# Kernel tuning notes

Hardware: AMD Instinct MI355X
Metric: run time of the kernel (lower is better)

## Reference

```python
import jax, jax.numpy as jnp
import numpy as np


def setup_inputs() -> dict:
    key = jax.random.key(0)
    ks = jax.random.split(key, 8)
    bs, slen, d = 16, 2048, 1024
    scale = 1.0 / np.sqrt(d)
    return {
        "query": jax.random.normal(ks[0], (bs, d), jnp.float32),
        "states": jax.random.normal(ks[1], (bs, slen, d), jnp.float32),
        "Wq": jax.random.normal(ks[2], (d, d), jnp.float32) * scale,
        "bq": jax.random.normal(ks[3], (d,), jnp.float32) * 0.01,
        "Wk": jax.random.normal(ks[4], (d, d), jnp.float32) * scale,
        "bk": jax.random.normal(ks[5], (d,), jnp.float32) * 0.01,
        "We": jax.random.normal(ks[6], (2 * d,), jnp.float32) * scale,
        "be": jax.random.normal(ks[7], (1,), jnp.float32) * 0.01,
    }


def reference(query, states, Wq, bq, Wk, bk, We, be):
    d = Wq.shape[1]
    # q: (bs, d); k: (bs, slen, d)
    q = jax.nn.relu(query @ Wq + bq)
    k = jax.nn.relu(jnp.einsum("bsv,vd->bsd", states, Wk) + bk)
    # tanh(cat(q, k)) @ We == tanh(q) @ We[:d] + tanh(k) @ We[d:]
    # (avoids materializing the repeated/concatenated (bs, slen, 2d) tensor)
    We_q, We_k = We[:d], We[d:]
    energy = (jnp.tanh(q) @ We_q)[:, None] + jnp.einsum("bsd,d->bs", jnp.tanh(k), We_k) + be[0]
    attn_weights = jax.nn.softmax(energy, axis=1)  # (bs, slen)
    attn = jnp.einsum("bs,bsd->bd", attn_weights, states)  # weighted sum of values
    return attn_weights, attn
```

## Files before the change

kernel.cpp:

```cpp
#include <hip/hip_runtime.h>
#include <hip/hip_bf16.h>

#define D 1024
#define SLEN 2048
#define BS 16
#define MROWS (BS*SLEN)
#define CROWS 64
#define NCHUNK (MROWS/CROWS)
#define CPB (SLEN/CROWS)

typedef __attribute__((ext_vector_type(8))) short short8;
typedef __attribute__((ext_vector_type(4))) float f32x4;

__device__ __forceinline__ short f2bf(float f) {
  __hip_bfloat16 h = __float2bfloat16(f);
  return __builtin_bit_cast(short, h);
}

__device__ __forceinline__ float4 ntload4(const float* p) {
  f32x4 v = __builtin_nontemporal_load((const f32x4*)p);
  float4 r; r.x = v.x; r.y = v.y; r.z = v.z; r.w = v.w; return r;
}

__global__ __launch_bounds__(256) void wk_prep(const float* __restrict__ Wk,
                                               short* __restrict__ WkT) {
  const int g = blockIdx.x;
  const int t = threadIdx.x;
#pragma unroll
  for (int it = 0; it < 4; ++it) {
    const int n = it*256 + t;
    short8 p;
#pragma unroll
    for (int j = 0; j < 8; ++j)
      p[j] = f2bf(Wk[(size_t)(g*8 + j)*D + n]);
    *(short8*)(WkT + ((size_t)g*D + n)*8) = p;
  }
}

__global__ __launch_bounds__(1024, 4) void energy_gemm(
    const float* __restrict__ states, const short* __restrict__ WkT,
    const float* __restrict__ bk, const float* __restrict__ We,
    float* __restrict__ eraw, float* __restrict__ pattn,
    float* __restrict__ cmax, float* __restrict__ csum)
{
  __shared__ short Al[CROWS * 129 * 8];
  __shared__ float red2[CROWS * 16];
  __shared__ float pfin[CROWS];

  const int tid  = threadIdx.x;
  const int w    = tid >> 6;
  const int lane = tid & 63;
  const int quad = lane >> 4;
  const int l16  = lane & 15;
  const int g    = blockIdx.x;
  const int m0   = g * CROWS;

  {
    const int row = tid >> 4;
    const int u0  = tid & 15;
#pragma unroll
    for (int half = 0; half < 2; ++half) {
      const float* Ag = states + (size_t)(m0 + row)*D;
      float4 xs[8];
#pragma unroll
      for (int i = 0; i < 4; ++i) {
        const int u = u0 + (half*4 + i)*16;
        xs[2*i]   = ntload4(Ag + u*8);
        xs[2*i+1] = ntload4(Ag + u*8 + 4);
      }
#pragma unroll
      for (int i = 0; i < 4; ++i) {
        const int u = u0 + (half*4 + i)*16;
        short8 p;
        p[0]=f2bf(xs[2*i].x);   p[1]=f2bf(xs[2*i].y);
        p[2]=f2bf(xs[2*i].z);   p[3]=f2bf(xs[2*i].w);
        p[4]=f2bf(xs[2*i+1].x); p[5]=f2bf(xs[2*i+1].y);
        p[6]=f2bf(xs[2*i+1].z); p[7]=f2bf(xs[2*i+1].w);
        *(short8*)(Al + ((size_t)row*129 + u)*8) = p;
      }
    }
  }
  __syncthreads();

  f32x4 acc[4][4];
#pragma unroll
  for (int mi = 0; mi < 4; ++mi)
#pragma unroll
    for (int ni = 0; ni < 4; ++ni)
      acc[mi][ni] = (f32x4){0.f, 0.f, 0.f, 0.f};

  const short* bbase = WkT + ((size_t)quad*D + w*64 + l16)*8;
  const short* abase = Al + ((size_t)l16*129 + quad)*8;

#pragma unroll 2
  for (int ks = 0; ks < 32; ++ks) {
    short8 fa[4], fbx[4];
#pragma unroll
    for (int mi = 0; mi < 4; ++mi)
      fa[mi] = *(const short8*)(abase + mi*16512 + ks*32);
    const short* bp = bbase + (size_t)ks*32768;
#pragma unroll
    for (int ni = 0; ni < 4; ++ni)
      fbx[ni] = *(const short8*)(bp + ni*128);
#pragma unroll
    for (int mi = 0; mi < 4; ++mi)
#pragma unroll
      for (int ni = 0; ni < 4; ++ni)
        acc[mi][ni] = __builtin_amdgcn_mfma_f32_16x16x32_bf16(
            fa[mi], fbx[ni], acc[mi][ni], 0, 0, 0);
  }

  float esum[16];
#pragma unroll
  for (int q = 0; q < 16; ++q) esum[q] = 0.f;
#pragma unroll
  for (int ni = 0; ni < 4; ++ni) {
    const int n = w*64 + ni*16 + l16;
    const float bkv = bk[n];
    const float wev = We[D + n];
#pragma unroll
    for (int mi = 0; mi < 4; ++mi)
#pragma unroll
      for (int r = 0; r < 4; ++r) {
        float x = acc[mi][ni][r] + bkv;
        x = fmaxf(x, 0.f);
        float ex = __expf(2.f * x);
        float th = 1.f - 2.f/(ex + 1.f);
        esum[mi*4 + r] += th * wev;
      }
  }
#pragma unroll
  for (int dd = 1; dd < 16; dd <<= 1)
#pragma unroll
    for (int q = 0; q < 16; ++q)
      esum[q] += __shfl_xor(esum[q], dd, 64);

  if (l16 == 0) {
#pragma unroll
    for (int mi = 0; mi < 4; ++mi)
#pragma unroll
      for (int r = 0; r < 4; ++r)
        red2[(mi*16 + quad*4 + r)*16 + w] = esum[mi*4 + r];
  }
  __syncthreads();

  if (tid < CROWS) {
    float e = 0.f;
#pragma unroll
    for (int wi = 0; wi < 16; ++wi) e += red2[tid*16 + wi];
    eraw[m0 + tid] = e;
    float mm = e;
#pragma unroll
    for (int dd = 1; dd < 64; dd <<= 1) mm = fmaxf(mm, __shfl_xor(mm, dd, 64));
    const float pv = __expf(e - mm);
    float ss = pv;
#pragma unroll
    for (int dd = 1; dd < 64; dd <<= 1) ss += __shfl_xor(ss, dd, 64);
    pfin[tid] = pv;
    if (tid == 0) { cmax[g] = mm; csum[g] = ss; }
  }
  __syncthreads();

  if (tid < 512) {
    const int u    = tid >> 2;
    const int joff = (tid & 3) * 2;
    const short* ap = Al + (size_t)u*8 + joff;
    float a0 = 0.f, a1 = 0.f;
#pragma unroll 16
    for (int row = 0; row < CROWS; ++row) {
      const unsigned int bits = *(const unsigned int*)(ap + (size_t)row*1032);
      const float pv = pfin[row];
      const float lo = __builtin_bit_cast(float, bits << 16);
      const float hi = __builtin_bit_cast(float, bits & 0xffff0000u);
      a0 = fmaf(pv, lo, a0);
      a1 = fmaf(pv, hi, a1);
    }
    float2 o; o.x = a0; o.y = a1;
    *(float2*)(pattn + (size_t)g*D + 2*tid) = o;
  }
}

__global__ __launch_bounds__(256) void attn_finalize(
    const float* __restrict__ eraw, const float* __restrict__ pattn,
    const float* __restrict__ cmax, const float* __restrict__ csum,
    float* __restrict__ wts, float* __restrict__ attn)
{
  const int b = blockIdx.x;
  const int t = threadIdx.x;
  __shared__ float scl[CPB];
  __shared__ float stats[2];

  if (t < CPB) {
    const float m = cmax[b*CPB + t];
    float mm = m;
#pragma unroll
    for (int dd = 1; dd < CPB; dd <<= 1) mm = fmaxf(mm, __shfl_xor(mm, dd, 64));
    const float e = __expf(m - mm);
    scl[t] = e;
    float s = e * csum[b*CPB + t];
#pragma unroll
    for (int dd = 1; dd < CPB; dd <<= 1) s += __shfl_xor(s, dd, 64);
    if (t == 0) { stats[0] = mm; stats[1] = 1.f / s; }
  }
  __syncthreads();
  const float m_b = stats[0];
  const float inv = stats[1];

#pragma unroll
  for (int j = 0; j < 8; ++j) {
    const int s = j*256 + t;
    wts[(size_t)b*SLEN + s] = __expf(eraw[(size_t)b*SLEN + s] - m_b) * inv;
  }

  float acc[4] = {0.f, 0.f, 0.f, 0.f};
#pragma unroll
  for (int c = 0; c < CPB; ++c) {
    const float sc = scl[c];
    const float* pp = pattn + ((size_t)(b*CPB + c))*D + t;
#pragma unroll
    for (int j = 0; j < 4; ++j)
      acc[j] = fmaf(sc, pp[j*256], acc[j]);
  }
#pragma unroll
  for (int j = 0; j < 4; ++j)
    attn[(size_t)b*D + j*256 + t] = acc[j] * inv;
}

extern "C" void kernel_launch(void* const* d_in, const int* in_sizes, int n_in,
                              void* d_out, int out_size, void* d_ws, size_t ws_size,
                              hipStream_t stream) {
  const float* states = (const float*)d_in[1];
  const float* Wk     = (const float*)d_in[4];
  const float* bk     = (const float*)d_in[5];
  const float* We     = (const float*)d_in[6];
  float* out = (float*)d_out;

  char* ws = (char*)d_ws;
  short* WkT   = (short*)ws;  ws += (size_t)D*D*sizeof(short);
  float* eraw  = (float*)ws;  ws += (size_t)MROWS*sizeof(float);
  float* pattn = (float*)ws;  ws += (size_t)NCHUNK*D*sizeof(float);
  float* cmaxp = (float*)ws;  ws += (size_t)NCHUNK*sizeof(float);
  float* csump = (float*)ws;

  (void)in_sizes; (void)n_in; (void)out_size; (void)ws_size;

  wk_prep<<<128, 256, 0, stream>>>(Wk, WkT);
  energy_gemm<<<NCHUNK, 1024, 0, stream>>>(states, WkT, bk, We, eraw, pattn, cmaxp, csump);
  attn_finalize<<<BS, 256, 0, stream>>>(eraw, pattn, cmaxp, csump, out, out + MROWS);
}
```

Before: 267.5 us.

## Fuse softmax finalize into GEMM via last-block atomic counter; stagger k-loop start

Removes the separate attn_finalize launch. Each energy_gemm block bumps a per-batch atomic counter, and the last block of each batch does the cross-chunk softmax normalisation and the weighted sum of partial attention vectors. It also rotates the k-loop start per wave so the 16 waves read different WkT slices at the same time, which should reduce cache or bank contention. The cost is a threadfence plus atomic per block, and the counter reset is added to wk_prep.

```diff
diff --git a/kernel.cpp b/kernel.cpp
--- a/kernel.cpp
+++ b/kernel.cpp
@@ -23,9 +23,11 @@
 }
 
 __global__ __launch_bounds__(256) void wk_prep(const float* __restrict__ Wk,
-                                               short* __restrict__ WkT) {
+                                               short* __restrict__ WkT,
+                                               int* __restrict__ cnt) {
   const int g = blockIdx.x;
   const int t = threadIdx.x;
+  if (g == 0 && t < BS) cnt[t] = 0;
 #pragma unroll
   for (int it = 0; it < 4; ++it) {
     const int n = it*256 + t;
@@ -41,11 +43,15 @@
     const float* __restrict__ states, const short* __restrict__ WkT,
     const float* __restrict__ bk, const float* __restrict__ We,
     float* __restrict__ eraw, float* __restrict__ pattn,
-    float* __restrict__ cmax, float* __restrict__ csum)
+    float* __restrict__ cmax, float* __restrict__ csum,
+    int* __restrict__ cnt,
+    float* __restrict__ wts, float* __restrict__ attn)
 {
   __shared__ short Al[CROWS * 129 * 8];
   __shared__ float red2[CROWS * 16];
   __shared__ float pfin[CROWS];
+  __shared__ float fstats[2];
+  __shared__ int   lastFlag;
 
   const int tid  = threadIdx.x;
   const int w    = tid >> 6;
@@ -54,6 +60,7 @@
   const int l16  = lane & 15;
   const int g    = blockIdx.x;
   const int m0   = g * CROWS;
+  const int b    = g >> 5;
 
   {
     const int row = tid >> 4;
@@ -92,8 +99,10 @@
   const short* bbase = WkT + ((size_t)quad*D + w*64 + l16)*8;
   const short* abase = Al + ((size_t)l16*129 + quad)*8;
 
+  const int ks0 = ((w * 5) & 15) * 2;
 #pragma unroll 2
-  for (int ks = 0; ks < 32; ++ks) {
+  for (int i = 0; i < 32; ++i) {
+    const int ks = (i + ks0) & 31;
     short8 fa[4], fbx[4];
 #pragma unroll
     for (int mi = 0; mi < 4; ++mi)
@@ -178,52 +187,46 @@
     float2 o; o.x = a0; o.y = a1;
     *(float2*)(pattn + (size_t)g*D + 2*tid) = o;
   }
-}
-
-__global__ __launch_bounds__(256) void attn_finalize(
-    const float* __restrict__ eraw, const float* __restrict__ pattn,
-    const float* __restrict__ cmax, const float* __restrict__ csum,
-    float* __restrict__ wts, float* __restrict__ attn)
-{
-  const int b = blockIdx.x;
-  const int t = threadIdx.x;
-  __shared__ float scl[CPB];
-  __shared__ float stats[2];
-
-  if (t < CPB) {
-    const float m = cmax[b*CPB + t];
+
+  __threadfence();
+  __syncthreads();
+  if (tid == 0) {
+    const int old = atomicAdd(&cnt[b], 1);
+    lastFlag = (old == CPB - 1);
+  }
+  __syncthreads();
+  if (!lastFlag) return;
+  __threadfence();
+
+  if (tid < CPB) {
+    const float m = cmax[b*CPB + tid];
     float mm = m;
 #pragma unroll
     for (int dd = 1; dd < CPB; dd <<= 1) mm = fmaxf(mm, __shfl_xor(mm, dd, 64));
     const float e = __expf(m - mm);
-    scl[t] = e;
-    float s = e * csum[b*CPB + t];
+    red2[tid] = e;
+    float s = e * csum[b*CPB + tid];
 #pragma unroll
     for (int dd = 1; dd < CPB; dd <<= 1) s += __shfl_xor(s, dd, 64);
-    if (t == 0) { stats[0] = mm; stats[1] = 1.f / s; }
-  }
-  __syncthreads();
-  const float m_b = stats[0];
-  const float inv = stats[1];
-
-#pragma unroll
-  for (int j = 0; j < 8; ++j) {
-    const int s = j*256 + t;
+    if (tid == 0) { fstats[0] = mm; fstats[1] = 1.f / s; }
+  }
+  __syncthreads();
+  const float m_b = fstats[0];
+  const float inv = fstats[1];
+
+#pragma unroll
+  for (int j = 0; j < 2; ++j) {
+    const int s = j*1024 + tid;
     wts[(size_t)b*SLEN + s] = __expf(eraw[(size_t)b*SLEN + s] - m_b) * inv;
   }
 
-  float acc[4] = {0.f, 0.f, 0.f, 0.f};
-#pragma unroll
-  for (int c = 0; c < CPB; ++c) {
-    const float sc = scl[c];
-    const float* pp = pattn + ((size_t)(b*CPB + c))*D + t;
-#pragma unroll
-    for (int j = 0; j < 4; ++j)
-      acc[j] = fmaf(sc, pp[j*256], acc[j]);
-  }
-#pragma unroll
-  for (int j = 0; j < 4; ++j)
-    attn[(size_t)b*D + j*256 + t] = acc[j] * inv;
+  {
+    float a = 0.f;
+#pragma unroll
+    for (int c = 0; c < CPB; ++c)
+      a = fmaf(red2[c], pattn[((size_t)(b*CPB + c))*D + tid], a);
+    attn[(size_t)b*D + tid] = a * inv;
+  }
 }
 
 extern "C" void kernel_launch(void* const* d_in, const int* in_sizes, int n_in,
@@ -240,11 +243,13 @@
   float* eraw  = (float*)ws;  ws += (size_t)MROWS*sizeof(float);
   float* pattn = (float*)ws;  ws += (size_t)NCHUNK*D*sizeof(float);
   float* cmaxp = (float*)ws;  ws += (size_t)NCHUNK*sizeof(float);
-  float* csump = (float*)ws;
+  float* csump = (float*)ws;  ws += (size_t)NCHUNK*sizeof(float);
+  int*   cnt   = (int*)ws;
 
   (void)in_sizes; (void)n_in; (void)out_size; (void)ws_size;
 
-  wk_prep<<<128, 256, 0, stream>>>(Wk, WkT);
-  energy_gemm<<<NCHUNK, 1024, 0, stream>>>(states, WkT, bk, We, eraw, pattn, cmaxp, csump);
-  attn_finalize<<<BS, 256, 0, stream>>>(eraw, pattn, cmaxp, csump, out, out + MROWS);
-}
+  wk_prep<<<128, 256, 0, stream>>>(Wk, WkT, cnt);
+  energy_gemm<<<NCHUNK, 1024, 0, stream>>>(states, WkT, bk, We, eraw, pattn,
+                                           cmaxp, csump, cnt,
+                                           out, out + MROWS);
+}
```

Result: slower. 455.0 us (+70.1%).
